# Optimization experiments

Hardware: AMD Instinct MI355X
Metric: run time of the kernel (lower is better)

## Reference

```python
import jax, jax.numpy as jnp
from jax import lax
import numpy as np

D = 56      # latent_rep_size
H = 501     # GRU hidden size
T = 277     # repeat length (sequence length)
O = 76      # fc2 output


def setup_inputs() -> dict:
    key = jax.random.key(0)
    ks = jax.random.split(key, 20)
    B = 256
    s = 0.05
    inp = {"x": jax.random.normal(ks[0], (B, D), dtype=jnp.float32)}
    inp["fc1_w"] = jax.random.normal(ks[1], (D, D), dtype=jnp.float32) * s
    inp["fc1_b"] = jax.random.normal(ks[2], (D,), dtype=jnp.float32) * s
    k = 3
    for l, in_dim in enumerate([D, H, H]):
        inp[f"w_ih{l}"] = jax.random.normal(ks[k], (3 * H, in_dim), dtype=jnp.float32) * s; k += 1
        inp[f"w_hh{l}"] = jax.random.normal(ks[k], (3 * H, H), dtype=jnp.float32) * s; k += 1
        inp[f"b_ih{l}"] = jax.random.normal(ks[k], (3 * H,), dtype=jnp.float32) * s; k += 1
        inp[f"b_hh{l}"] = jax.random.normal(ks[k], (3 * H,), dtype=jnp.float32) * s; k += 1
    inp["fc2_w"] = jax.random.normal(ks[k], (O, H), dtype=jnp.float32) * s; k += 1
    inp["fc2_b"] = jax.random.normal(ks[k], (O,), dtype=jnp.float32) * s
    return inp


def _gru_step(h, g, w_hh, b_hh):
    # g: precomputed input gates (B, 3H) in PyTorch order [r, z, n]
    hg = h @ w_hh.T + b_hh                       # (B, 3H)
    r = jax.nn.sigmoid(g[:, :H] + hg[:, :H])
    z = jax.nn.sigmoid(g[:, H:2 * H] + hg[:, H:2 * H])
    n = jnp.tanh(g[:, 2 * H:] + r * hg[:, 2 * H:])
    h_new = (1.0 - z) * n + z * h
    return h_new, h_new


def _gru_layer(x_gates, w_hh, b_hh, B, dtype):
    # x_gates: (T, B, 3H) input contribution per timestep
    h0 = jnp.zeros((B, H), dtype)
    _, ys = lax.scan(lambda h, g: _gru_step(h, g, w_hh, b_hh), h0, x_gates)
    return ys  # (T, B, H)


def reference(x, fc1_w, fc1_b,
              w_ih0, w_hh0, b_ih0, b_hh0,
              w_ih1, w_hh1, b_ih1, b_hh1,
              w_ih2, w_hh2, b_ih2, b_hh2,
              fc2_w, fc2_b):
    B = x.shape[0]
    dtype = x.dtype
    # fc1 + relu, then the input is repeated 277 times -> layer-0 input gates
    # are identical at every timestep; compute them once (B, 3H).
    h_in = jax.nn.relu(x @ fc1_w.T + fc1_b)             # (B, D)
    g0 = h_in @ w_ih0.T + b_ih0                          # (B, 3H), constant over t
    h0 = jnp.zeros((B, H), dtype)
    _, ys0 = lax.scan(lambda h, _: _gru_step(h, g0, w_hh0, b_hh0), h0, None, length=T)
    # layers 1 and 2: precompute input gates for all timesteps, then scan
    g1 = jnp.einsum('tbh,gh->tbg', ys0, w_ih1) + b_ih1   # (T, B, 3H)
    ys1 = _gru_layer(g1, w_hh1, b_hh1, B, dtype)
    g2 = jnp.einsum('tbh,gh->tbg', ys1, w_ih2) + b_ih2
    ys2 = _gru_layer(g2, w_hh2, b_hh2, B, dtype)
    # fc2 then permute(1, 2, 0): (T, B, O) -> (B, O, T)
    out = jnp.einsum('tbh,oh->tbo', ys2, fc2_w) + fc2_b
    return jnp.transpose(out, (1, 2, 0))
```

## Files before the change

kernel.cpp:

```cpp
#include <hip/hip_runtime.h>
#include <hip/hip_bf16.h>
#include <math.h>

#define D_IN 56
#define H    501
#define T_STEPS 277
#define O_OUT 76
#define BATCH 256
#define HP   512
#define NP   1504
#define SSTR 520
#define HSTR 576

#define LDS_SA    0
#define LDS_SB    (32 * SSTR)
#define LDS_SC    (64 * SSTR)
#define LDS_STAGE (96 * SSTR)
#define DYN_LDS   (96 * SSTR * 2 + 18 * HSTR * 4 + 32 * 48 * 4 + 3 * 4 * 16 * 4)

typedef __attribute__((ext_vector_type(8))) short s16x8;
typedef __attribute__((ext_vector_type(4))) float f32x4;
typedef unsigned long long ull;

__device__ __forceinline__ short f2bf(float x) {
    union { float f; unsigned u; } v; v.f = x;
    unsigned r = (v.u + 0x7fffu + ((v.u >> 16) & 1u)) >> 16;
    return (short)r;
}
__device__ __forceinline__ float bf2f(short b) {
    union { unsigned u; float f; } v; v.u = ((unsigned)(unsigned short)b) << 16;
    return v.f;
}
__device__ __forceinline__ float sigm(float x) { return 1.f / (1.f + __expf(-x)); }
__device__ __forceinline__ float tanh_fast(float x) { return 1.f - 2.f / (1.f + __expf(2.f * x)); }

__global__ void k_pack_gru(const float* __restrict__ w_ih,
                           const float* __restrict__ w_hh,
                           short* __restrict__ dst, int KT) {
    int tile = blockIdx.x;
    int ktp  = tile % KT;
    int g    = (tile / KT) % 3;
    int j    = tile / (KT * 3);
    int l    = threadIdx.x;
    int u    = j * 16 + (l & 15);
    int row  = g * H + u;
    const float* src; int k0;
    if (KT == 32) {
        if (ktp < 16) { src = w_ih; k0 = ktp * 32; }
        else          { src = w_hh; k0 = (ktp - 16) * 32; }
    } else          { src = w_hh; k0 = ktp * 32; }
    k0 += (l >> 4) * 8;
    short* p = dst + ((size_t)tile * 64 + l) * 8;
    for (int jj = 0; jj < 8; jj++) {
        int k = k0 + jj;
        float v = 0.f;
        if (u < H && k < H) v = src[(size_t)row * H + k];
        p[jj] = f2bf(v);
    }
}

__global__ void k_pack_fc2(const float* __restrict__ w, short* __restrict__ dst) {
    int tile = blockIdx.x;
    int kt = tile % 16, mt = tile / 16;
    int l = threadIdx.x;
    int o = mt * 16 + (l & 15);
    int k0 = kt * 32 + (l >> 4) * 8;
    short* p = dst + ((size_t)tile * 64 + l) * 8;
    for (int jj = 0; jj < 8; jj++) {
        int k = k0 + jj; float v = 0.f;
        if (o < O_OUT && k < H) v = w[(size_t)o * H + k];
        p[jj] = f2bf(v);
    }
}

__global__ void k_hin(const float* __restrict__ x, const float* __restrict__ w,
                      const float* __restrict__ bias, float* __restrict__ hin) {
    int b = blockIdx.x, o = threadIdx.x;
    float acc = 0.f;
    if (o < D_IN) {
        acc = bias[o];
        for (int k = 0; k < D_IN; k++) acc += x[b * D_IN + k] * w[o * D_IN + k];
        acc = fmaxf(acc, 0.f);
    }
    hin[b * 64 + o] = (o < D_IN) ? acc : 0.f;
}

__global__ void k_g0(const float* __restrict__ hin, const float* __restrict__ w_ih0,
                     const float* __restrict__ b_ih0, float* __restrict__ g0) {
    int b = blockIdx.x, tid = threadIdx.x;
    __shared__ float shx[D_IN];
    if (tid < D_IN) shx[tid] = hin[b * 64 + tid];
    __syncthreads();
    for (int o = tid; o < NP; o += 256) {
        float acc = 0.f;
        if (o < 3 * H) {
            acc = b_ih0[o];
            for (int k = 0; k < D_IN; k++) acc += shx[k] * w_ih0[(size_t)o * D_IN + k];
        }
        g0[(size_t)b * NP + o] = acc;
    }
}

template <int NK>
__device__ __forceinline__ void role_mfma(const short* __restrict__ stg, int abase, int ak0,
                                          const short* __restrict__ wg0,
                                          const short* __restrict__ wg1,
                                          const short* __restrict__ wg2,
                                          float* __restrict__ dr, float* __restrict__ dz,
                                          float* __restrict__ dn, int lane) {
    const int arow = lane & 15;
    const int acol = (lane >> 4) * 8;
    f32x4 ar0 = {0.f,0.f,0.f,0.f}, ar1 = {0.f,0.f,0.f,0.f};
    f32x4 az0 = {0.f,0.f,0.f,0.f}, az1 = {0.f,0.f,0.f,0.f};
    f32x4 an0 = {0.f,0.f,0.f,0.f}, an1 = {0.f,0.f,0.f,0.f};
    #pragma unroll
    for (int kk = 0; kk < NK; kk++) {
        int ak = ak0 + kk;
        s16x8 x0 = *(const s16x8*)&stg[abase + arow * SSTR + ak * 32 + acol];
        s16x8 x1 = *(const s16x8*)&stg[abase + (16 + arow) * SSTR + ak * 32 + acol];
        s16x8 br = *(const s16x8*)&wg0[(size_t)kk * 512 + lane * 8];
        s16x8 bz = *(const s16x8*)&wg1[(size_t)kk * 512 + lane * 8];
        s16x8 bn = *(const s16x8*)&wg2[(size_t)kk * 512 + lane * 8];
        ar0 = __builtin_amdgcn_mfma_f32_16x16x32_bf16(x0, br, ar0, 0, 0, 0);
        ar1 = __builtin_amdgcn_mfma_f32_16x16x32_bf16(x1, br, ar1, 0, 0, 0);
        az0 = __builtin_amdgcn_mfma_f32_16x16x32_bf16(x0, bz, az0, 0, 0, 0);
        az1 = __builtin_amdgcn_mfma_f32_16x16x32_bf16(x1, bz, az1, 0, 0, 0);
        an0 = __builtin_amdgcn_mfma_f32_16x16x32_bf16(x0, bn, an0, 0, 0, 0);
        an1 = __builtin_amdgcn_mfma_f32_16x16x32_bf16(x1, bn, an1, 0, 0, 0);
    }
    int ul = lane & 15, mrow = (lane >> 4) * 4;
    #pragma unroll
    for (int r = 0; r < 4; r++) {
        dr[(mrow + r) * 18 + ul]      = ar0[r];
        dr[(16 + mrow + r) * 18 + ul] = ar1[r];
        dz[(mrow + r) * 18 + ul]      = az0[r];
        dz[(16 + mrow + r) * 18 + ul] = az1[r];
        dn[(mrow + r) * 18 + ul]      = an0[r];
        dn[(16 + mrow + r) * 18 + ul] = an1[r];
    }
}

__global__ __launch_bounds__(384, 1)
void k_gru_persist(const short* __restrict__ packW0,
                   const short* __restrict__ packW1,
                   const short* __restrict__ packW2,
                   const float* __restrict__ g0,
                   const float* __restrict__ b_hh0,
                   const float* __restrict__ b_ih1, const float* __restrict__ b_hh1,
                   const float* __restrict__ b_ih2, const float* __restrict__ b_hh2,
                   short* __restrict__ ysA,
                   short* __restrict__ ysB,
                   unsigned* __restrict__ cnt) {
    const int bg   = blockIdx.x >> 5;
    const int j    = ((blockIdx.x & 7) << 2) | ((blockIdx.x >> 3) & 3);
    const int b0   = bg * 32;
    const int tid  = threadIdx.x;
    const int lane = tid & 63;
    const int wave = tid >> 6;
    const s16x8 z8 = {0, 0, 0, 0, 0, 0, 0, 0};

    extern __shared__ __align__(16) char smem[];
    short* stg = (short*)smem;
    float* hgl = (float*)(smem + LDS_STAGE * 2);
    float* sg0 = hgl + 18 * HSTR;
    float* sbb = sg0 + 32 * 48;

    int abase, ak0, slot0;
    const short* wg0; const short* wg1; const short* wg2;
    {
        const short* wpk; int KT, kt0;
        switch (wave) {
            case 0:  wpk = packW0; KT = 16; kt0 = 0;  abase = LDS_SA; ak0 = 0; slot0 = 0;  break;
            case 1:  wpk = packW0; KT = 16; kt0 = 8;  abase = LDS_SA; ak0 = 8; slot0 = 1;  break;
            case 2:  wpk = packW1; KT = 32; kt0 = 0;  abase = LDS_SA; ak0 = 0; slot0 = 6;  break;
            case 3:  wpk = packW1; KT = 32; kt0 = 16; abase = LDS_SB; ak0 = 0; slot0 = 7;  break;
            case 4:  wpk = packW2; KT = 32; kt0 = 0;  abase = LDS_SB; ak0 = 0; slot0 = 12; break;
            default: wpk = packW2; KT = 32; kt0 = 16; abase = LDS_SC; ak0 = 0; slot0 = 13; break;
        }
        wg0 = wpk + ((size_t)((j * 3 + 0) * KT + kt0) * 512);
        wg1 = wpk + ((size_t)((j * 3 + 1) * KT + kt0) * 512);
        wg2 = wpk + ((size_t)((j * 3 + 2) * KT + kt0) * 512);
    }
    float* dr = hgl + (size_t)slot0 * HSTR;
    float* dz = hgl + (size_t)(slot0 + 2) * HSTR;
    float* dn = hgl + (size_t)(slot0 + 4) * HSTR;

    for (int c = tid; c < 32 * 48; c += 384) {
        int m = c / 48, col = c % 48;
        int g = col >> 4, ul = col & 15;
        int u = j * 16 + ul;
        float v = 0.f;
        if (u < H) {
            v = g0[(size_t)(b0 + m) * NP + g * H + u];
            if (g == 0) v += b_hh0[u];
            else if (g == 1) v += b_hh0[H + u];
        }
        sg0[m * 48 + col] = v;
    }
    if (tid < 48) {
        int l = tid >> 4, ul = tid & 15, u = j * 16 + ul;
        float br = 0.f, bz = 0.f, bxn = 0.f, bhn = 0.f;
        if (u < H) {
            if (l == 0) bhn = b_hh0[2 * H + u];
            else {
                const float* bi = (l == 1) ? b_ih1 : b_ih2;
                const float* bh = (l == 1) ? b_hh1 : b_hh2;
                br = bi[u] + bh[u]; bz = bi[H + u] + bh[H + u];
                bxn = bi[2 * H + u]; bhn = bh[2 * H + u];
            }
        }
        sbb[(l * 4 + 0) * 16 + ul] = br;  sbb[(l * 4 + 1) * 16 + ul] = bz;
        sbb[(l * 4 + 2) * 16 + ul] = bxn; sbb[(l * 4 + 3) * 16 + ul] = bhn;
    }
    __syncthreads();

    unsigned* mycnt = cnt + bg * 32;

    for (int s = 0; s < T_STEPS + 2; ++s) {
        const bool hasL0 = (s < T_STEPS);
        const bool hasL1 = (s >= 1 && s <= T_STEPS);
        const bool hasL2 = (s >= 2);
        const short* ysAm1 = ysA + (size_t)(s - 1) * BATCH * HP;
        const short* ysBm2 = ysB + (size_t)(s - 2) * BATCH * HP;
        const short* ysAm3 = ysA + (size_t)(s - 3) * BATCH * HP;

        #pragma unroll
        for (int i = 0; i < 6; i++) {
            int c = tid + i * 384;
            if (c < 2048) {
                int r = c >> 6, cc = c & 63;
                size_t goff = (size_t)(b0 + r) * HP + cc * 8;
                s16x8 va = z8, vb = z8, vc = z8;
                if (s >= 1 && s <= T_STEPS) va = *(const s16x8*)&ysAm1[goff];
                if (s >= 2)                 vb = *(const s16x8*)&ysBm2[goff];
                if (s >= 3) {
                    const ull* p = (const ull*)&ysAm3[goff];
                    union { ull q[2]; s16x8 v; } uu;
                    uu.q[0] = __hip_atomic_load(p,     __ATOMIC_RELAXED, __HIP_MEMORY_SCOPE_AGENT);
                    uu.q[1] = __hip_atomic_load(p + 1, __ATOMIC_RELAXED, __HIP_MEMORY_SCOPE_AGENT);
                    vc = uu.v;
                }
                int loff = r * SSTR + cc * 8;
                *(s16x8*)&stg[LDS_SA + loff] = va;
                *(s16x8*)&stg[LDS_SB + loff] = vb;
                *(s16x8*)&stg[LDS_SC + loff] = vc;
            }
        }
        __syncthreads();

        {
            const bool active = (wave < 2) ? hasL0 : ((wave < 4) ? hasL1 : hasL2);
            if (active) {
                if (wave < 2) role_mfma<8>(stg, abase, ak0, wg0, wg1, wg2, dr, dz, dn, lane);
                else          role_mfma<16>(stg, abase, ak0, wg0, wg1, wg2, dr, dz, dn, lane);
            }
        }
        __syncthreads();

        #pragma unroll
        for (int it = 0; it < 2; it++) {
            int idx = tid + it * 384;
            int which = idx >> 8, id8 = idx & 255;
            int m = id8 >> 3, pr = id8 & 7;
            int b = b0 + m;
            if (which == 0 && hasL0) {
                short* dst = ysA + (size_t)s * BATCH * HP;
                unsigned pk = 0;
                #pragma unroll
                for (int e = 0; e < 2; e++) {
                    int ul = pr * 2 + e, u = j * 16 + ul, mo = m * 18 + ul;
                    float hv = 0.f;
                    if (u < H) {
                        float hr = hgl[0 * HSTR + mo] + hgl[1 * HSTR + mo];
                        float hz = hgl[2 * HSTR + mo] + hgl[3 * HSTR + mo];
                        float hn = hgl[4 * HSTR + mo] + hgl[5 * HSTR + mo];
                        float r = sigm(sg0[m * 48 + ul] + hr);
                        float z = sigm(sg0[m * 48 + 16 + ul] + hz);
                        float n = tanh_fast(sg0[m * 48 + 32 + ul] + r * (hn + sbb[3 * 16 + ul]));
                        float hold = bf2f(stg[LDS_SA + m * SSTR + u]);
                        hv = (1.f - z) * n + z * hold;
                    }
                    pk |= ((unsigned)(unsigned short)f2bf(hv)) << (16 * e);
                }
                __hip_atomic_store((unsigned*)&dst[(size_t)b * HP + j * 16 + pr * 2], pk,
                                   __ATOMIC_RELAXED, __HIP_MEMORY_SCOPE_AGENT);
            } else if (which == 1 && hasL1) {
                short* dst = ysB + (size_t)(s - 1) * BATCH * HP;
                unsigned pk = 0;
                #pragma unroll
                for (int e = 0; e < 2; e++) {
                    int ul = pr * 2 + e, u = j * 16 + ul, mo = m * 18 + ul;
                    float hv = 0.f;
                    if (u < H) {
                        float xr = hgl[6 * HSTR + mo]  + sbb[(4 + 0) * 16 + ul];
                        float hr = hgl[7 * HSTR + mo];
                        float xz = hgl[8 * HSTR + mo]  + sbb[(4 + 1) * 16 + ul];
                        float hz = hgl[9 * HSTR + mo];
                        float xn = hgl[10 * HSTR + mo] + sbb[(4 + 2) * 16 + ul];
                        float hn = hgl[11 * HSTR + mo] + sbb[(4 + 3) * 16 + ul];
                        float r = sigm(xr + hr);
                        float z = sigm(xz + hz);
                        float n = tanh_fast(xn + r * hn);
                        float hold = bf2f(stg[LDS_SB + m * SSTR + u]);
                        hv = (1.f - z) * n + z * hold;
                    }
                    pk |= ((unsigned)(unsigned short)f2bf(hv)) << (16 * e);
                }
                __hip_atomic_store((unsigned*)&dst[(size_t)b * HP + j * 16 + pr * 2], pk,
                                   __ATOMIC_RELAXED, __HIP_MEMORY_SCOPE_AGENT);
            } else if (which == 2 && hasL2) {
                short* dst = ysA + (size_t)(s - 2) * BATCH * HP;
                unsigned pk = 0;
                #pragma unroll
                for (int e = 0; e < 2; e++) {
                    int ul = pr * 2 + e, u = j * 16 + ul, mo = m * 18 + ul;
                    float hv = 0.f;
                    if (u < H) {
                        float xr = hgl[12 * HSTR + mo] + sbb[(8 + 0) * 16 + ul];
                        float hr = hgl[13 * HSTR + mo];
                        float xz = hgl[14 * HSTR + mo] + sbb[(8 + 1) * 16 + ul];
                        float hz = hgl[15 * HSTR + mo];
                        float xn = hgl[16 * HSTR + mo] + sbb[(8 + 2) * 16 + ul];
                        float hn = hgl[17 * HSTR + mo] + sbb[(8 + 3) * 16 + ul];
                        float r = sigm(xr + hr);
                        float z = sigm(xz + hz);
                        float n = tanh_fast(xn + r * hn);
                        float hold = bf2f(stg[LDS_SC + m * SSTR + u]);
                        hv = (1.f - z) * n + z * hold;
                    }
                    pk |= ((unsigned)(unsigned short)f2bf(hv)) << (16 * e);
                }
                __hip_atomic_store((unsigned*)&dst[(size_t)b * HP + j * 16 + pr * 2], pk,
                                   __ATOMIC_RELAXED, __HIP_MEMORY_SCOPE_AGENT);
            }
        }
        __syncthreads();

        if (tid == 0) {
            asm volatile("s_waitcnt vmcnt(0)" ::: "memory");
            __hip_atomic_fetch_add(mycnt, 1u, __ATOMIC_RELAXED, __HIP_MEMORY_SCOPE_AGENT);
            unsigned tgt = 32u * (unsigned)(s + 1);
            while (__hip_atomic_load(mycnt, __ATOMIC_RELAXED, __HIP_MEMORY_SCOPE_AGENT) < tgt) {}
        }
        __syncthreads();
    }
}

__global__ __launch_bounds__(256, 1)
void k_fc2(const short* __restrict__ ys2, const short* __restrict__ fc2p,
           const float* __restrict__ fc2_b, float* __restrict__ out) {
    int b = blockIdx.x;
    int tid = threadIdx.x, lane = tid & 63, wave = tid >> 6;
    const s16x8 zf = {0, 0, 0, 0, 0, 0, 0, 0};
    for (int ntile = wave; ntile < 18; ntile += 4) {
        int tt = ntile * 16 + (lane & 15);
        s16x8 bf[16];
        for (int kt = 0; kt < 16; kt++) {
            if (tt < T_STEPS)
                bf[kt] = *(const s16x8*)&ys2[((size_t)tt * BATCH + b) * HP + kt * 32 + (lane >> 4) * 8];
            else
                bf[kt] = zf;
        }
        for (int mt = 0; mt < 5; mt++) {
            f32x4 acc = {0.f, 0.f, 0.f, 0.f};
            for (int kt = 0; kt < 16; kt++) {
                s16x8 af = *(const s16x8*)&fc2p[(((size_t)mt * 16 + kt) * 64 + lane) * 8];
                acc = __builtin_amdgcn_mfma_f32_16x16x32_bf16(af, bf[kt], acc, 0, 0, 0);
            }
            int obase = mt * 16 + (lane >> 4) * 4;
            for (int r = 0; r < 4; r++) {
                int o = obase + r;
                if (o < O_OUT && tt < T_STEPS)
                    out[((size_t)b * O_OUT + o) * T_STEPS + tt] = acc[r] + fc2_b[o];
            }
        }
    }
}

extern "C" void kernel_launch(void* const* d_in, const int* in_sizes, int n_in,
                              void* d_out, int out_size, void* d_ws, size_t ws_size,
                              hipStream_t stream) {
    const float* x     = (const float*)d_in[0];
    const float* fc1_w = (const float*)d_in[1];
    const float* fc1_b = (const float*)d_in[2];
    const float* w_ih0 = (const float*)d_in[3];
    const float* w_hh0 = (const float*)d_in[4];
    const float* b_ih0 = (const float*)d_in[5];
    const float* b_hh0 = (const float*)d_in[6];
    const float* w_ih1 = (const float*)d_in[7];
    const float* w_hh1 = (const float*)d_in[8];
    const float* b_ih1 = (const float*)d_in[9];
    const float* b_hh1 = (const float*)d_in[10];
    const float* w_ih2 = (const float*)d_in[11];
    const float* w_hh2 = (const float*)d_in[12];
    const float* b_ih2 = (const float*)d_in[13];
    const float* b_hh2 = (const float*)d_in[14];
    const float* fc2_w = (const float*)d_in[15];
    const float* fc2_b = (const float*)d_in[16];
    float* out = (float*)d_out;

    char* p = (char*)d_ws;
    auto alloc = [&](size_t bytes) {
        char* r = p; p += (bytes + 255) & ~(size_t)255; return r;
    };
    short* packW0 = (short*)alloc((size_t)32 * 3 * 16 * 64 * 8 * 2);
    short* packW1 = (short*)alloc((size_t)32 * 3 * 32 * 64 * 8 * 2);
    short* packW2 = (short*)alloc((size_t)32 * 3 * 32 * 64 * 8 * 2);
    short* packF  = (short*)alloc((size_t)80 * 64 * 8 * 2);
    float* hin    = (float*)alloc((size_t)BATCH * 64 * 4);
    float* g0     = (float*)alloc((size_t)BATCH * NP * 4);
    unsigned* cnt = (unsigned*)alloc(256 * 4);
    short* ysA    = (short*)alloc((size_t)T_STEPS * BATCH * HP * 2);
    short* ysB    = (short*)alloc((size_t)T_STEPS * BATCH * HP * 2);

    static bool attr_set = false;
    if (!attr_set) {
        (void)hipFuncSetAttribute((const void*)k_gru_persist,
                                  hipFuncAttributeMaxDynamicSharedMemorySize,
                                  DYN_LDS);
        attr_set = true;
    }

    hipMemsetAsync(cnt, 0, 256 * 4, stream);
    k_pack_gru<<<32 * 3 * 16, 64, 0, stream>>>(nullptr, w_hh0, packW0, 16);
    k_pack_gru<<<32 * 3 * 32, 64, 0, stream>>>(w_ih1, w_hh1, packW1, 32);
    k_pack_gru<<<32 * 3 * 32, 64, 0, stream>>>(w_ih2, w_hh2, packW2, 32);
    k_pack_fc2<<<80, 64, 0, stream>>>(fc2_w, packF);
    k_hin<<<BATCH, 64, 0, stream>>>(x, fc1_w, fc1_b, hin);
    k_g0<<<BATCH, 256, 0, stream>>>(hin, w_ih0, b_ih0, g0);

    k_gru_persist<<<256, 384, DYN_LDS, stream>>>(packW0, packW1, packW2, g0,
                                                 b_hh0, b_ih1, b_hh1, b_ih2, b_hh2,
                                                 ysA, ysB, cnt);

    k_fc2<<<BATCH, 256, 0, stream>>>(ysA, packF, fc2_b, out);
}
```

Before: 2.423 ms.

## Keep recurrent weight fragments resident in registers across GRU timesteps

Each wave now loads its slice of the packed recurrent weights into a 48-entry register array once before the time loop, instead of re-reading them from global memory at every timestep in the MFMA loop. The launch bound changes to allow two blocks per CU, and the block-to-(batch group, unit tile) mapping is reordered. This removes repeated global/L2 weight traffic on the serial critical path. The cost is heavy VGPR pressure (384 registers for weights alone), which risks spills, especially under the tighter 2-blocks-per-CU bound.

```diff
diff --git a/kernel.cpp b/kernel.cpp
--- a/kernel.cpp
+++ b/kernel.cpp
@@ -102,12 +102,10 @@
 }
 
 template <int NK>
-__device__ __forceinline__ void role_mfma(const short* __restrict__ stg, int abase, int ak0,
-                                          const short* __restrict__ wg0,
-                                          const short* __restrict__ wg1,
-                                          const short* __restrict__ wg2,
-                                          float* __restrict__ dr, float* __restrict__ dz,
-                                          float* __restrict__ dn, int lane) {
+__device__ __forceinline__ void role_mfma_reg(const short* __restrict__ stg, int abase, int ak0,
+                                              const s16x8 (&wv)[48],
+                                              float* __restrict__ dr, float* __restrict__ dz,
+                                              float* __restrict__ dn, int lane) {
     const int arow = lane & 15;
     const int acol = (lane >> 4) * 8;
     f32x4 ar0 = {0.f,0.f,0.f,0.f}, ar1 = {0.f,0.f,0.f,0.f};
@@ -118,15 +116,12 @@
         int ak = ak0 + kk;
         s16x8 x0 = *(const s16x8*)&stg[abase + arow * SSTR + ak * 32 + acol];
         s16x8 x1 = *(const s16x8*)&stg[abase + (16 + arow) * SSTR + ak * 32 + acol];
-        s16x8 br = *(const s16x8*)&wg0[(size_t)kk * 512 + lane * 8];
-        s16x8 bz = *(const s16x8*)&wg1[(size_t)kk * 512 + lane * 8];
-        s16x8 bn = *(const s16x8*)&wg2[(size_t)kk * 512 + lane * 8];
-        ar0 = __builtin_amdgcn_mfma_f32_16x16x32_bf16(x0, br, ar0, 0, 0, 0);
-        ar1 = __builtin_amdgcn_mfma_f32_16x16x32_bf16(x1, br, ar1, 0, 0, 0);
-        az0 = __builtin_amdgcn_mfma_f32_16x16x32_bf16(x0, bz, az0, 0, 0, 0);
-        az1 = __builtin_amdgcn_mfma_f32_16x16x32_bf16(x1, bz, az1, 0, 0, 0);
-        an0 = __builtin_amdgcn_mfma_f32_16x16x32_bf16(x0, bn, an0, 0, 0, 0);
-        an1 = __builtin_amdgcn_mfma_f32_16x16x32_bf16(x1, bn, an1, 0, 0, 0);
+        ar0 = __builtin_amdgcn_mfma_f32_16x16x32_bf16(x0, wv[3 * kk + 0], ar0, 0, 0, 0);
+        ar1 = __builtin_amdgcn_mfma_f32_16x16x32_bf16(x1, wv[3 * kk + 0], ar1, 0, 0, 0);
+        az0 = __builtin_amdgcn_mfma_f32_16x16x32_bf16(x0, wv[3 * kk + 1], az0, 0, 0, 0);
+        az1 = __builtin_amdgcn_mfma_f32_16x16x32_bf16(x1, wv[3 * kk + 1], az1, 0, 0, 0);
+        an0 = __builtin_amdgcn_mfma_f32_16x16x32_bf16(x0, wv[3 * kk + 2], an0, 0, 0, 0);
+        an1 = __builtin_amdgcn_mfma_f32_16x16x32_bf16(x1, wv[3 * kk + 2], an1, 0, 0, 0);
     }
     int ul = lane & 15, mrow = (lane >> 4) * 4;
     #pragma unroll
@@ -140,7 +135,7 @@
     }
 }
 
-__global__ __launch_bounds__(384, 1)
+__global__ __launch_bounds__(384, 2)
 void k_gru_persist(const short* __restrict__ packW0,
                    const short* __restrict__ packW1,
                    const short* __restrict__ packW2,
@@ -151,8 +146,8 @@
                    short* __restrict__ ysA,
                    short* __restrict__ ysB,
                    unsigned* __restrict__ cnt) {
-    const int bg   = blockIdx.x >> 5;
-    const int j    = ((blockIdx.x & 7) << 2) | ((blockIdx.x >> 3) & 3);
+    const int bg   = blockIdx.x & 7;
+    const int j    = blockIdx.x >> 3;
     const int b0   = bg * 32;
     const int tid  = threadIdx.x;
     const int lane = tid & 63;
@@ -166,7 +161,7 @@
     float* sbb = sg0 + 32 * 48;
 
     int abase, ak0, slot0;
-    const short* wg0; const short* wg1; const short* wg2;
+    s16x8 wv[48];
     {
         const short* wpk; int KT, kt0;
         switch (wave) {
@@ -177,9 +172,24 @@
             case 4:  wpk = packW2; KT = 32; kt0 = 0;  abase = LDS_SB; ak0 = 0; slot0 = 12; break;
             default: wpk = packW2; KT = 32; kt0 = 16; abase = LDS_SC; ak0 = 0; slot0 = 13; break;
         }
-        wg0 = wpk + ((size_t)((j * 3 + 0) * KT + kt0) * 512);
-        wg1 = wpk + ((size_t)((j * 3 + 1) * KT + kt0) * 512);
-        wg2 = wpk + ((size_t)((j * 3 + 2) * KT + kt0) * 512);
+        const short* wg0 = wpk + ((size_t)((j * 3 + 0) * KT + kt0) * 512);
+        const short* wg1 = wpk + ((size_t)((j * 3 + 1) * KT + kt0) * 512);
+        const short* wg2 = wpk + ((size_t)((j * 3 + 2) * KT + kt0) * 512);
+        if (wave < 2) {
+            #pragma unroll
+            for (int kk = 0; kk < 8; kk++) {
+                wv[3 * kk + 0] = *(const s16x8*)&wg0[(size_t)kk * 512 + lane * 8];
+                wv[3 * kk + 1] = *(const s16x8*)&wg1[(size_t)kk * 512 + lane * 8];
+                wv[3 * kk + 2] = *(const s16x8*)&wg2[(size_t)kk * 512 + lane * 8];
+            }
+        } else {
+            #pragma unroll
+            for (int kk = 0; kk < 16; kk++) {
+                wv[3 * kk + 0] = *(const s16x8*)&wg0[(size_t)kk * 512 + lane * 8];
+                wv[3 * kk + 1] = *(const s16x8*)&wg1[(size_t)kk * 512 + lane * 8];
+                wv[3 * kk + 2] = *(const s16x8*)&wg2[(size_t)kk * 512 + lane * 8];
+            }
+        }
     }
     float* dr = hgl + (size_t)slot0 * HSTR;
     float* dz = hgl + (size_t)(slot0 + 2) * HSTR;
@@ -251,8 +261,8 @@
         {
             const bool active = (wave < 2) ? hasL0 : ((wave < 4) ? hasL1 : hasL2);
             if (active) {
-                if (wave < 2) role_mfma<8>(stg, abase, ak0, wg0, wg1, wg2, dr, dz, dn, lane);
-                else          role_mfma<16>(stg, abase, ak0, wg0, wg1, wg2, dr, dz, dn, lane);
+                if (wave < 2) role_mfma_reg<8>(stg, abase, ak0, wv, dr, dz, dn, lane);
+                else          role_mfma_reg<16>(stg, abase, ak0, wv, dr, dz, dn, lane);
             }
         }
         __syncthreads();
```

After: 2.265 ms, median of 2. 6.5% less time.

## Split GRU gate MFMA work across ten waves per block instead of six

Applied to the files above, without the earlier changes.

Each persistent block now runs 640 threads (10 waves) instead of 384. Each role's three gate matmuls are split between two waves: one does the r gate plus the first half of z, the other does the second half of z plus n. This shortens the per-wave serial MFMA chain on the recurrent critical path. It also remaps blockIdx to (bg, j) differently, adds two LDS slots for the partial z sums, and changes launch bounds to (640,2), which may pressure registers.

```diff
diff --git a/kernel.cpp b/kernel.cpp
--- a/kernel.cpp
+++ b/kernel.cpp
@@ -11,12 +11,13 @@
 #define NP   1504
 #define SSTR 520
 #define HSTR 576
+#define NSLOT 20
 
 #define LDS_SA    0
 #define LDS_SB    (32 * SSTR)
 #define LDS_SC    (64 * SSTR)
 #define LDS_STAGE (96 * SSTR)
-#define DYN_LDS   (96 * SSTR * 2 + 18 * HSTR * 4 + 32 * 48 * 4 + 3 * 4 * 16 * 4)
+#define DYN_LDS   (96 * SSTR * 2 + NSLOT * HSTR * 4 + 32 * 48 * 4 + 3 * 4 * 16 * 4)
 
 typedef __attribute__((ext_vector_type(8))) short s16x8;
 typedef __attribute__((ext_vector_type(4))) float f32x4;
@@ -101,46 +102,47 @@
     }
 }
 
-template <int NK>
-__device__ __forceinline__ void role_mfma(const short* __restrict__ stg, int abase, int ak0,
-                                          const short* __restrict__ wg0,
-                                          const short* __restrict__ wg1,
-                                          const short* __restrict__ wg2,
-                                          float* __restrict__ dr, float* __restrict__ dz,
-                                          float* __restrict__ dn, int lane) {
+template <int NKA, int NKB>
+__device__ __forceinline__ void role2(const short* __restrict__ stg, int abase,
+                                      const short* __restrict__ wA, int akA0,
+                                      const short* __restrict__ wB, int akB0,
+                                      float* __restrict__ dA, float* __restrict__ dB,
+                                      int lane) {
     const int arow = lane & 15;
     const int acol = (lane >> 4) * 8;
-    f32x4 ar0 = {0.f,0.f,0.f,0.f}, ar1 = {0.f,0.f,0.f,0.f};
-    f32x4 az0 = {0.f,0.f,0.f,0.f}, az1 = {0.f,0.f,0.f,0.f};
-    f32x4 an0 = {0.f,0.f,0.f,0.f}, an1 = {0.f,0.f,0.f,0.f};
+    f32x4 aA0 = {0.f,0.f,0.f,0.f}, aA1 = {0.f,0.f,0.f,0.f};
+    f32x4 aB0 = {0.f,0.f,0.f,0.f}, aB1 = {0.f,0.f,0.f,0.f};
+    constexpr int NKM = (NKA > NKB) ? NKA : NKB;
     #pragma unroll
-    for (int kk = 0; kk < NK; kk++) {
-        int ak = ak0 + kk;
-        s16x8 x0 = *(const s16x8*)&stg[abase + arow * SSTR + ak * 32 + acol];
-        s16x8 x1 = *(const s16x8*)&stg[abase + (16 + arow) * SSTR + ak * 32 + acol];
-        s16x8 br = *(const s16x8*)&wg0[(size_t)kk * 512 + lane * 8];
-        s16x8 bz = *(const s16x8*)&wg1[(size_t)kk * 512 + lane * 8];
-        s16x8 bn = *(const s16x8*)&wg2[(size_t)kk * 512 + lane * 8];
-        ar0 = __builtin_amdgcn_mfma_f32_16x16x32_bf16(x0, br, ar0, 0, 0, 0);
-        ar1 = __builtin_amdgcn_mfma_f32_16x16x32_bf16(x1, br, ar1, 0, 0, 0);
-        az0 = __builtin_amdgcn_mfma_f32_16x16x32_bf16(x0, bz, az0, 0, 0, 0);
-        az1 = __builtin_amdgcn_mfma_f32_16x16x32_bf16(x1, bz, az1, 0, 0, 0);
-        an0 = __builtin_amdgcn_mfma_f32_16x16x32_bf16(x0, bn, an0, 0, 0, 0);
-        an1 = __builtin_amdgcn_mfma_f32_16x16x32_bf16(x1, bn, an1, 0, 0, 0);
-    }
-    int ul = lane & 15, mrow = (lane >> 4) * 4;
+    for (int kk = 0; kk < NKM; kk++) {
+        if (kk < NKA) {
+            s16x8 w = *(const s16x8*)&wA[(size_t)kk * 512 + lane * 8];
+            int ak = akA0 + kk;
+            s16x8 x0 = *(const s16x8*)&stg[abase + arow * SSTR + ak * 32 + acol];
+            s16x8 x1 = *(const s16x8*)&stg[abase + (16 + arow) * SSTR + ak * 32 + acol];
+            aA0 = __builtin_amdgcn_mfma_f32_16x16x32_bf16(x0, w, aA0, 0, 0, 0);
+            aA1 = __builtin_amdgcn_mfma_f32_16x16x32_bf16(x1, w, aA1, 0, 0, 0);
+        }
+        if (kk < NKB) {
+            s16x8 w = *(const s16x8*)&wB[(size_t)kk * 512 + lane * 8];
+            int ak = akB0 + kk;
+            s16x8 x0 = *(const s16x8*)&stg[abase + arow * SSTR + ak * 32 + acol];
+            s16x8 x1 = *(const s16x8*)&stg[abase + (16 + arow) * SSTR + ak * 32 + acol];
+            aB0 = __builtin_amdgcn_mfma_f32_16x16x32_bf16(x0, w, aB0, 0, 0, 0);
+            aB1 = __builtin_amdgcn_mfma_f32_16x16x32_bf16(x1, w, aB1, 0, 0, 0);
+        }
+    }
+    const int ul = lane & 15, mrow = (lane >> 4) * 4;
     #pragma unroll
     for (int r = 0; r < 4; r++) {
-        dr[(mrow + r) * 18 + ul]      = ar0[r];
-        dr[(16 + mrow + r) * 18 + ul] = ar1[r];
-        dz[(mrow + r) * 18 + ul]      = az0[r];
-        dz[(16 + mrow + r) * 18 + ul] = az1[r];
-        dn[(mrow + r) * 18 + ul]      = an0[r];
-        dn[(16 + mrow + r) * 18 + ul] = an1[r];
-    }
-}
-
-__global__ __launch_bounds__(384, 1)
+        dA[(mrow + r) * 18 + ul]      = aA0[r];
+        dA[(16 + mrow + r) * 18 + ul] = aA1[r];
+        dB[(mrow + r) * 18 + ul]      = aB0[r];
+        dB[(16 + mrow + r) * 18 + ul] = aB1[r];
+    }
+}
+
+__global__ __launch_bounds__(640, 2)
 void k_gru_persist(const short* __restrict__ packW0,
                    const short* __restrict__ packW1,
                    const short* __restrict__ packW2,
@@ -151,8 +153,8 @@
                    short* __restrict__ ysA,
                    short* __restrict__ ysB,
                    unsigned* __restrict__ cnt) {
-    const int bg   = blockIdx.x >> 5;
-    const int j    = ((blockIdx.x & 7) << 2) | ((blockIdx.x >> 3) & 3);
+    const int bg   = blockIdx.x & 7;
+    const int j    = blockIdx.x >> 3;
     const int b0   = bg * 32;
     const int tid  = threadIdx.x;
     const int lane = tid & 63;
@@ -162,30 +164,26 @@
     extern __shared__ __align__(16) char smem[];
     short* stg = (short*)smem;
     float* hgl = (float*)(smem + LDS_STAGE * 2);
-    float* sg0 = hgl + 18 * HSTR;
+    float* sg0 = hgl + NSLOT * HSTR;
     float* sbb = sg0 + 32 * 48;
 
-    int abase, ak0, slot0;
-    const short* wg0; const short* wg1; const short* wg2;
-    {
-        const short* wpk; int KT, kt0;
-        switch (wave) {
-            case 0:  wpk = packW0; KT = 16; kt0 = 0;  abase = LDS_SA; ak0 = 0; slot0 = 0;  break;
-            case 1:  wpk = packW0; KT = 16; kt0 = 8;  abase = LDS_SA; ak0 = 8; slot0 = 1;  break;
-            case 2:  wpk = packW1; KT = 32; kt0 = 0;  abase = LDS_SA; ak0 = 0; slot0 = 6;  break;
-            case 3:  wpk = packW1; KT = 32; kt0 = 16; abase = LDS_SB; ak0 = 0; slot0 = 7;  break;
-            case 4:  wpk = packW2; KT = 32; kt0 = 0;  abase = LDS_SB; ak0 = 0; slot0 = 12; break;
-            default: wpk = packW2; KT = 32; kt0 = 16; abase = LDS_SC; ak0 = 0; slot0 = 13; break;
-        }
-        wg0 = wpk + ((size_t)((j * 3 + 0) * KT + kt0) * 512);
-        wg1 = wpk + ((size_t)((j * 3 + 1) * KT + kt0) * 512);
-        wg2 = wpk + ((size_t)((j * 3 + 2) * KT + kt0) * 512);
-    }
-    float* dr = hgl + (size_t)slot0 * HSTR;
-    float* dz = hgl + (size_t)(slot0 + 2) * HSTR;
-    float* dn = hgl + (size_t)(slot0 + 4) * HSTR;
-
-    for (int c = tid; c < 32 * 48; c += 384) {
+    const int grp = wave >> 1;
+    const int sub = wave & 1;
+    int abase;
+    const short* wpk; int KT, kt0;
+    switch (grp) {
+        case 0:  wpk = packW0; KT = 16; kt0 = 0;  abase = LDS_SA; break;
+        case 1:  wpk = packW1; KT = 32; kt0 = 0;  abase = LDS_SA; break;
+        case 2:  wpk = packW1; KT = 32; kt0 = 16; abase = LDS_SB; break;
+        case 3:  wpk = packW2; KT = 32; kt0 = 0;  abase = LDS_SB; break;
+        default: wpk = packW2; KT = 32; kt0 = 16; abase = LDS_SC; break;
+    }
+    const short* wr = wpk + ((size_t)((j * 3 + 0) * KT + kt0) * 512);
+    const short* wz = wpk + ((size_t)((j * 3 + 1) * KT + kt0) * 512);
+    const short* wn = wpk + ((size_t)((j * 3 + 2) * KT + kt0) * 512);
+    float* slotb = hgl + (size_t)(4 * grp) * HSTR;
+
+    for (int c = tid; c < 32 * 48; c += 640) {
         int m = c / 48, col = c % 48;
         int g = col >> 4, ul = col & 15;
         int u = j * 16 + ul;
@@ -224,42 +222,40 @@
         const short* ysBm2 = ysB + (size_t)(s - 2) * BATCH * HP;
         const short* ysAm3 = ysA + (size_t)(s - 3) * BATCH * HP;
 
-        #pragma unroll
-        for (int i = 0; i < 6; i++) {
-            int c = tid + i * 384;
-            if (c < 2048) {
-                int r = c >> 6, cc = c & 63;
-                size_t goff = (size_t)(b0 + r) * HP + cc * 8;
-                s16x8 va = z8, vb = z8, vc = z8;
-                if (s >= 1 && s <= T_STEPS) va = *(const s16x8*)&ysAm1[goff];
-                if (s >= 2)                 vb = *(const s16x8*)&ysBm2[goff];
-                if (s >= 3) {
-                    const ull* p = (const ull*)&ysAm3[goff];
-                    union { ull q[2]; s16x8 v; } uu;
-                    uu.q[0] = __hip_atomic_load(p,     __ATOMIC_RELAXED, __HIP_MEMORY_SCOPE_AGENT);
-                    uu.q[1] = __hip_atomic_load(p + 1, __ATOMIC_RELAXED, __HIP_MEMORY_SCOPE_AGENT);
-                    vc = uu.v;
-                }
-                int loff = r * SSTR + cc * 8;
-                *(s16x8*)&stg[LDS_SA + loff] = va;
-                *(s16x8*)&stg[LDS_SB + loff] = vb;
-                *(s16x8*)&stg[LDS_SC + loff] = vc;
-            }
+        for (int c = tid; c < 2048; c += 640) {
+            int r = c >> 6, cc = c & 63;
+            size_t goff = (size_t)(b0 + r) * HP + cc * 8;
+            s16x8 va = z8, vb = z8, vc = z8;
+            if (s >= 1 && s <= T_STEPS) va = *(const s16x8*)&ysAm1[goff];
+            if (s >= 2)                 vb = *(const s16x8*)&ysBm2[goff];
+            if (s >= 3) {
+                const ull* p = (const ull*)&ysAm3[goff];
+                union { ull q[2]; s16x8 v; } uu;
+                uu.q[0] = __hip_atomic_load(p,     __ATOMIC_RELAXED, __HIP_MEMORY_SCOPE_AGENT);
+                uu.q[1] = __hip_atomic_load(p + 1, __ATOMIC_RELAXED, __HIP_MEMORY_SCOPE_AGENT);
+                vc = uu.v;
+            }
+            int loff = r * SSTR + cc * 8;
+            *(s16x8*)&stg[LDS_SA + loff] = va;
+            *(s16x8*)&stg[LDS_SB + loff] = vb;
+            *(s16x8*)&stg[LDS_SC + loff] = vc;
         }
         __syncthreads();
 
         {
-            const bool active = (wave < 2) ? hasL0 : ((wave < 4) ? hasL1 : hasL2);
+            const bool active = (grp == 0) ? hasL0 : ((grp < 3) ? hasL1 : hasL2);
             if (active) {
-                if (wave < 2) role_mfma<8>(stg, abase, ak0, wg0, wg1, wg2, dr, dz, dn, lane);
-                else          role_mfma<16>(stg, abase, ak0, wg0, wg1, wg2, dr, dz, dn, lane);
+                if (sub == 0)
+                    role2<16, 8>(stg, abase, wr, 0, wz, 0,
+                                 slotb + 0 * HSTR, slotb + 1 * HSTR, lane);
+                else
+                    role2<8, 16>(stg, abase, wz + (size_t)8 * 512, 8, wn, 0,
+                                 slotb + 2 * HSTR, slotb + 3 * HSTR, lane);
             }
         }
         __syncthreads();
 
-        #pragma unroll
-        for (int it = 0; it < 2; it++) {
-            int idx = tid + it * 384;
+        for (int idx = tid; idx < 768; idx += 640) {
             int which = idx >> 8, id8 = idx & 255;
             int m = id8 >> 3, pr = id8 & 7;
             int b = b0 + m;
@@ -271,9 +267,9 @@
                     int ul = pr * 2 + e, u = j * 16 + ul, mo = m * 18 + ul;
                     float hv = 0.f;
                     if (u < H) {
-                        float hr = hgl[0 * HSTR + mo] + hgl[1 * HSTR + mo];
-                        float hz = hgl[2 * HSTR + mo] + hgl[3 * HSTR + mo];
-                        float hn = hgl[4 * HSTR + mo] + hgl[5 * HSTR + mo];
+                        float hr = hgl[0 * HSTR + mo];
+                        float hz = hgl[1 * HSTR + mo] + hgl[2 * HSTR + mo];
+                        float hn = hgl[3 * HSTR + mo];
                         float r = sigm(sg0[m * 48 + ul] + hr);
                         float z = sigm(sg0[m * 48 + 16 + ul] + hz);
                         float n = tanh_fast(sg0[m * 48 + 32 + ul] + r * (hn + sbb[3 * 16 + ul]));
@@ -292,11 +288,11 @@
                     int ul = pr * 2 + e, u = j * 16 + ul, mo = m * 18 + ul;
                     float hv = 0.f;
                     if (u < H) {
-                        float xr = hgl[6 * HSTR + mo]  + sbb[(4 + 0) * 16 + ul];
-                        float hr = hgl[7 * HSTR + mo];
-                        float xz = hgl[8 * HSTR + mo]  + sbb[(4 + 1) * 16 + ul];
-                        float hz = hgl[9 * HSTR + mo];
-                        float xn = hgl[10 * HSTR + mo] + sbb[(4 + 2) * 16 + ul];
+                        float xr = hgl[4 * HSTR + mo] + sbb[(4 + 0) * 16 + ul];
+                        float xz = hgl[5 * HSTR + mo] + hgl[6 * HSTR + mo] + sbb[(4 + 1) * 16 + ul];
+                        float xn = hgl[7 * HSTR + mo] + sbb[(4 + 2) * 16 + ul];
+                        float hr = hgl[8 * HSTR + mo];
+                        float hz = hgl[9 * HSTR + mo] + hgl[10 * HSTR + mo];
                         float hn = hgl[11 * HSTR + mo] + sbb[(4 + 3) * 16 + ul];
                         float r = sigm(xr + hr);
                         float z = sigm(xz + hz);
@@ -317,11 +313,11 @@
                     float hv = 0.f;
                     if (u < H) {
                         float xr = hgl[12 * HSTR + mo] + sbb[(8 + 0) * 16 + ul];
-                        float hr = hgl[13 * HSTR + mo];
-                        float xz = hgl[14 * HSTR + mo] + sbb[(8 + 1) * 16 + ul];
-                        float hz = hgl[15 * HSTR + mo];
-                        float xn = hgl[16 * HSTR + mo] + sbb[(8 + 2) * 16 + ul];
-                        float hn = hgl[17 * HSTR + mo] + sbb[(8 + 3) * 16 + ul];
+                        float xz = hgl[13 * HSTR + mo] + hgl[14 * HSTR + mo] + sbb[(8 + 1) * 16 + ul];
+                        float xn = hgl[15 * HSTR + mo] + sbb[(8 + 2) * 16 + ul];
+                        float hr = hgl[16 * HSTR + mo];
+                        float hz = hgl[17 * HSTR + mo] + hgl[18 * HSTR + mo];
+                        float hn = hgl[19 * HSTR + mo] + sbb[(8 + 3) * 16 + ul];
                         float r = sigm(xr + hr);
                         float z = sigm(xz + hz);
                         float n = tanh_fast(xn + r * hn);
@@ -429,7 +425,7 @@
     k_hin<<<BATCH, 64, 0, stream>>>(x, fc1_w, fc1_b, hin);
     k_g0<<<BATCH, 256, 0, stream>>>(hin, w_ih0, b_ih0, g0);
 
-    k_gru_persist<<<256, 384, DYN_LDS, stream>>>(packW0, packW1, packW2, g0,
+    k_gru_persist<<<256, 640, DYN_LDS, stream>>>(packW0, packW1, packW2, g0,
                                                  b_hh0, b_ih1, b_hh1, b_ih2, b_hh2,
                                                  ysA, ysB, cnt);
 
```

Measured after the change: 4.155 ms. +71.5%, slower.

## Split each GRU role across two waves by batch-row halves, 768 threads

Applied to the files above, without the earlier changes.

Doubles the block to 12 waves so each MFMA role is shared by two waves, each handling 16 of the 32 batch rows. This halves the serial MFMA chain per wave on the recurrent critical path, and the staging and gate loops are redistributed over the larger thread count. The block-to-(batch group, hidden tile) mapping also changes, so consecutive block IDs now cover different batch groups. In exchange each wave loads the same B-fragment weights redundantly, and every step needs more waves to synchronise.

```diff
diff --git a/kernel.cpp b/kernel.cpp
--- a/kernel.cpp
+++ b/kernel.cpp
@@ -102,45 +102,39 @@
 }
 
 template <int NK>
-__device__ __forceinline__ void role_mfma(const short* __restrict__ stg, int abase, int ak0,
+__device__ __forceinline__ void role_half(const short* __restrict__ stg, int abase, int ak0,
+                                          int rowoff,
                                           const short* __restrict__ wg0,
                                           const short* __restrict__ wg1,
                                           const short* __restrict__ wg2,
                                           float* __restrict__ dr, float* __restrict__ dz,
                                           float* __restrict__ dn, int lane) {
-    const int arow = lane & 15;
+    const int arow = rowoff + (lane & 15);
     const int acol = (lane >> 4) * 8;
-    f32x4 ar0 = {0.f,0.f,0.f,0.f}, ar1 = {0.f,0.f,0.f,0.f};
-    f32x4 az0 = {0.f,0.f,0.f,0.f}, az1 = {0.f,0.f,0.f,0.f};
-    f32x4 an0 = {0.f,0.f,0.f,0.f}, an1 = {0.f,0.f,0.f,0.f};
+    f32x4 ar0 = {0.f,0.f,0.f,0.f};
+    f32x4 az0 = {0.f,0.f,0.f,0.f};
+    f32x4 an0 = {0.f,0.f,0.f,0.f};
     #pragma unroll
     for (int kk = 0; kk < NK; kk++) {
         int ak = ak0 + kk;
         s16x8 x0 = *(const s16x8*)&stg[abase + arow * SSTR + ak * 32 + acol];
-        s16x8 x1 = *(const s16x8*)&stg[abase + (16 + arow) * SSTR + ak * 32 + acol];
         s16x8 br = *(const s16x8*)&wg0[(size_t)kk * 512 + lane * 8];
         s16x8 bz = *(const s16x8*)&wg1[(size_t)kk * 512 + lane * 8];
         s16x8 bn = *(const s16x8*)&wg2[(size_t)kk * 512 + lane * 8];
         ar0 = __builtin_amdgcn_mfma_f32_16x16x32_bf16(x0, br, ar0, 0, 0, 0);
-        ar1 = __builtin_amdgcn_mfma_f32_16x16x32_bf16(x1, br, ar1, 0, 0, 0);
         az0 = __builtin_amdgcn_mfma_f32_16x16x32_bf16(x0, bz, az0, 0, 0, 0);
-        az1 = __builtin_amdgcn_mfma_f32_16x16x32_bf16(x1, bz, az1, 0, 0, 0);
         an0 = __builtin_amdgcn_mfma_f32_16x16x32_bf16(x0, bn, an0, 0, 0, 0);
-        an1 = __builtin_amdgcn_mfma_f32_16x16x32_bf16(x1, bn, an1, 0, 0, 0);
-    }
-    int ul = lane & 15, mrow = (lane >> 4) * 4;
+    }
+    int ul = lane & 15, mrow = rowoff + (lane >> 4) * 4;
     #pragma unroll
     for (int r = 0; r < 4; r++) {
-        dr[(mrow + r) * 18 + ul]      = ar0[r];
-        dr[(16 + mrow + r) * 18 + ul] = ar1[r];
-        dz[(mrow + r) * 18 + ul]      = az0[r];
-        dz[(16 + mrow + r) * 18 + ul] = az1[r];
-        dn[(mrow + r) * 18 + ul]      = an0[r];
-        dn[(16 + mrow + r) * 18 + ul] = an1[r];
-    }
-}
-
-__global__ __launch_bounds__(384, 1)
+        dr[(mrow + r) * 18 + ul] = ar0[r];
+        dz[(mrow + r) * 18 + ul] = az0[r];
+        dn[(mrow + r) * 18 + ul] = an0[r];
+    }
+}
+
+__global__ __launch_bounds__(768, 3)
 void k_gru_persist(const short* __restrict__ packW0,
                    const short* __restrict__ packW1,
                    const short* __restrict__ packW2,
@@ -151,12 +145,14 @@
                    short* __restrict__ ysA,
                    short* __restrict__ ysB,
                    unsigned* __restrict__ cnt) {
-    const int bg   = blockIdx.x >> 5;
-    const int j    = ((blockIdx.x & 7) << 2) | ((blockIdx.x >> 3) & 3);
+    const int bg   = blockIdx.x & 7;
+    const int j    = blockIdx.x >> 3;
     const int b0   = bg * 32;
     const int tid  = threadIdx.x;
     const int lane = tid & 63;
     const int wave = tid >> 6;
+    const int pair = wave >> 1;
+    const int half = wave & 1;
     const s16x8 z8 = {0, 0, 0, 0, 0, 0, 0, 0};
 
     extern __shared__ __align__(16) char smem[];
@@ -169,7 +165,7 @@
     const short* wg0; const short* wg1; const short* wg2;
     {
         const short* wpk; int KT, kt0;
-        switch (wave) {
+        switch (pair) {
             case 0:  wpk = packW0; KT = 16; kt0 = 0;  abase = LDS_SA; ak0 = 0; slot0 = 0;  break;
             case 1:  wpk = packW0; KT = 16; kt0 = 8;  abase = LDS_SA; ak0 = 8; slot0 = 1;  break;
             case 2:  wpk = packW1; KT = 32; kt0 = 0;  abase = LDS_SA; ak0 = 0; slot0 = 6;  break;
@@ -184,8 +180,9 @@
     float* dr = hgl + (size_t)slot0 * HSTR;
     float* dz = hgl + (size_t)(slot0 + 2) * HSTR;
     float* dn = hgl + (size_t)(slot0 + 4) * HSTR;
-
-    for (int c = tid; c < 32 * 48; c += 384) {
+    const int rowoff = half * 16;
+
+    for (int c = tid; c < 32 * 48; c += 768) {
         int m = c / 48, col = c % 48;
         int g = col >> 4, ul = col & 15;
         int u = j * 16 + ul;
@@ -225,8 +222,8 @@
         const short* ysAm3 = ysA + (size_t)(s - 3) * BATCH * HP;
 
         #pragma unroll
-        for (int i = 0; i < 6; i++) {
-            int c = tid + i * 384;
+        for (int i = 0; i < 3; i++) {
+            int c = tid + i * 768;
             if (c < 2048) {
                 int r = c >> 6, cc = c & 63;
                 size_t goff = (size_t)(b0 + r) * HP + cc * 8;
@@ -249,17 +246,16 @@
         __syncthreads();
 
         {
-            const bool active = (wave < 2) ? hasL0 : ((wave < 4) ? hasL1 : hasL2);
+            const bool active = (pair < 2) ? hasL0 : ((pair < 4) ? hasL1 : hasL2);
             if (active) {
-                if (wave < 2) role_mfma<8>(stg, abase, ak0, wg0, wg1, wg2, dr, dz, dn, lane);
-                else          role_mfma<16>(stg, abase, ak0, wg0, wg1, wg2, dr, dz, dn, lane);
+                if (pair < 2) role_half<8>(stg, abase, ak0, rowoff, wg0, wg1, wg2, dr, dz, dn, lane);
+                else          role_half<16>(stg, abase, ak0, rowoff, wg0, wg1, wg2, dr, dz, dn, lane);
             }
         }
         __syncthreads();
 
-        #pragma unroll
-        for (int it = 0; it < 2; it++) {
-            int idx = tid + it * 384;
+        {
+            int idx = tid;
             int which = idx >> 8, id8 = idx & 255;
             int m = id8 >> 3, pr = id8 & 7;
             int b = b0 + m;
@@ -429,7 +425,7 @@
     k_hin<<<BATCH, 64, 0, stream>>>(x, fc1_w, fc1_b, hin);
     k_g0<<<BATCH, 256, 0, stream>>>(hin, w_ih0, b_ih0, g0);
 
-    k_gru_persist<<<256, 384, DYN_LDS, stream>>>(packW0, packW1, packW2, g0,
+    k_gru_persist<<<256, 768, DYN_LDS, stream>>>(packW0, packW1, packW2, g0,
                                                  b_hh0, b_ih1, b_hh1, b_ih2, b_hh2,
                                                  ysA, ysB, cnt);
 
```

After: 3.845 ms. +58.7%, slower.
